# Performance work log

Measured on AMD Instinct MI355X. Metric: run time of the kernel, lower is better.

## Reference

```python
import jax, jax.numpy as jnp
import numpy as np

N_NODES = 100000
N_EDGES = 1600000
IN_DIM, HID_DIM, OUT_DIM = 128, 64, 64


def setup_inputs() -> dict:
    key = jax.random.key(0)
    ks = jax.random.split(key, 8)
    x = jax.random.normal(ks[0], (N_NODES, IN_DIM), dtype=jnp.float32)
    edge_index = jax.random.randint(ks[1], (2, N_EDGES), 0, N_NODES, dtype=jnp.int32)
    edge_weight = jax.random.uniform(ks[2], (N_EDGES,), dtype=jnp.float32)
    # GCNConv parameters (glorot-ish init)
    w1 = jax.random.normal(ks[3], (IN_DIM, HID_DIM), dtype=jnp.float32) / np.sqrt(IN_DIM)
    b1 = jnp.zeros((HID_DIM,), dtype=jnp.float32)
    w2 = jax.random.normal(ks[4], (HID_DIM, OUT_DIM), dtype=jnp.float32) / np.sqrt(HID_DIM)
    b2 = jnp.zeros((OUT_DIM,), dtype=jnp.float32)
    return {"x": x, "edge_index": edge_index, "edge_weight": edge_weight,
            "w1": w1, "b1": b1, "w2": w2, "b2": b2}


def _gcn_conv(h, src, dst, edge_weight, w, b, n_nodes):
    # GCNConv(normalize=False): linear transform, then edge-weighted scatter-add
    # (source_to_target flow: gather from src, scatter-sum into dst), then bias.
    h = h @ w                                   # [N, out]
    msg = h[src] * edge_weight[:, None]          # [E, out] irregular gather
    agg = jax.ops.segment_sum(msg, dst, num_segments=n_nodes)  # [N, out]
    return agg + b


def reference(x, edge_index, edge_weight, w1, b1, w2, b2):
    src, dst = edge_index[0], edge_index[1]
    n = x.shape[0]
    # Dropout is identity in eval mode (training=False).
    h = _gcn_conv(x, src, dst, edge_weight, w1, b1, n)
    h = jax.nn.relu(h)
    out = _gcn_conv(h, src, dst, edge_weight, w2, b2, n)
    return out
```

## Files before the change

### kernel.cpp

```cpp
#include <hip/hip_runtime.h>
#include <hip/hip_bf16.h>


#define N_NODES 100000
#define N_EDGES 1600000
#define NB1     391
#define T1      4096
#define NT1     391
#define CAP1    4706
#define GB1     782

typedef unsigned short ushort_t;
typedef unsigned int uint_t;
typedef __attribute__((ext_vector_type(8))) short bf16x8;
typedef __attribute__((ext_vector_type(4))) float floatx4;
typedef __attribute__((ext_vector_type(8))) ushort_t ushort8v;

static __device__ __forceinline__ float bf2f(ushort_t h) {
    return __uint_as_float(((uint_t)h) << 16);
}
static __device__ __forceinline__ ushort_t f2bf(float f) {
    uint_t u = __float_as_uint(f);
    u = (u + 0x7FFF + ((u >> 16) & 1)) >> 16;
    return (ushort_t)u;
}

__global__ __launch_bounds__(512) void k_init(int* __restrict__ gcursor)
{
    int t = threadIdx.x;
    if (t < NB1) gcursor[t] = t * CAP1;
}

__global__ __launch_bounds__(512) void k_p1g1(
    const int* __restrict__ src, const int* __restrict__ dst,
    const float* __restrict__ ew, int* __restrict__ gcursor,
    int2* __restrict__ recs1, int E,
    const float* __restrict__ X, const float* __restrict__ W,
    ushort_t* __restrict__ Y, int N)
{
    __shared__ __align__(16) char smem[52224];
    const int tid = threadIdx.x;

    if (blockIdx.x < NT1) {
        int* cnt     = (int*)smem;
        int* start   = cnt + NB1;
        int* cursor  = start + NB1;
        int* gb      = cursor + NB1;
        int* s       = (int*)(smem + 6256);
        int2* stg    = (int2*)(smem + 8304);
        ushort_t* sb = (ushort_t*)(smem + 41072);
        const int t = tid, b = blockIdx.x;

        if (t < NB1) cnt[t] = 0;
        __syncthreads();
        const int e0 = b * T1;
        const int e1 = min(E, e0 + T1);
        for (int e = e0 + t; e < e1; e += 512)
            atomicAdd(&cnt[dst[e] >> 8], 1);
        __syncthreads();
        const int v = (t < NB1) ? cnt[t] : 0;
        s[t] = v;
        #pragma unroll
        for (int off = 1; off < 512; off <<= 1) {
            __syncthreads();
            int a = (t >= off) ? s[t - off] : 0;
            __syncthreads();
            s[t] += a;
        }
        __syncthreads();
        if (t < NB1) {
            int st = s[t] - v;
            start[t]  = st;
            cursor[t] = st;
            gb[t]     = atomicAdd(&gcursor[t], v);
        }
        __syncthreads();
        for (int e = e0 + t; e < e1; e += 512) {
            int d  = dst[e];
            int bk = d >> 8;
            int p  = atomicAdd(&cursor[bk], 1);
            int2 r;
            r.x = ((d & 255) << 17) | src[e];
            r.y = __float_as_int(ew[e]);
            stg[p] = r;
            sb[p]  = (ushort_t)bk;
        }
        __syncthreads();
        const int n = e1 - e0;
        for (int i = t; i < n; i += 512) {
            int bk = sb[i];
            recs1[gb[bk] + (i - start[bk])] = stg[i];
        }
    } else {
        ushort_t* sA = (ushort_t*)smem;
        ushort_t* sB = (ushort_t*)(smem + 34816);
        const int b    = blockIdx.x - NT1;
        const int row0 = b * 128;

        for (int i = tid; i < 128 * 32; i += 512) {
            int r = i >> 5, c4 = (i & 31) * 4;
            int rg = row0 + r; if (rg > N - 1) rg = N - 1;
            float4 v = *(const float4*)(X + (size_t)rg * 128 + c4);
            ushort4 pk = make_ushort4(f2bf(v.x), f2bf(v.y), f2bf(v.z), f2bf(v.w));
            *(ushort4*)(sA + r * 136 + c4) = pk;
        }
        for (int i = tid; i < 128 * 16; i += 512) {
            int k = i >> 4, n4 = (i & 15) * 4;
            float4 v = *(const float4*)(W + (size_t)k * 64 + n4);
            sB[(n4 + 0) * 136 + k] = f2bf(v.x);
            sB[(n4 + 1) * 136 + k] = f2bf(v.y);
            sB[(n4 + 2) * 136 + k] = f2bf(v.z);
            sB[(n4 + 3) * 136 + k] = f2bf(v.w);
        }
        __syncthreads();

        const int wid = tid >> 6, lane = tid & 63;
        const int m = lane & 15, quad = lane >> 4;
        floatx4 acc[4] = {};

        #pragma unroll
        for (int ks = 0; ks < 4; ++ks) {
            bf16x8 a = *(const bf16x8*)(sA + (wid * 16 + m) * 136 + ks * 32 + quad * 8);
            #pragma unroll
            for (int nt = 0; nt < 4; ++nt) {
                bf16x8 bfr = *(const bf16x8*)(sB + (nt * 16 + m) * 136 + ks * 32 + quad * 8);
                acc[nt] = __builtin_amdgcn_mfma_f32_16x16x32_bf16(a, bfr, acc[nt], 0, 0, 0);
            }
        }
        __syncthreads();
        #pragma unroll
        for (int nt = 0; nt < 4; ++nt)
            #pragma unroll
            for (int r = 0; r < 4; ++r)
                sA[(wid * 16 + quad * 4 + r) * 72 + nt * 16 + m] = f2bf(acc[nt][r]);
        __syncthreads();
        for (int i = tid; i < 128 * 8; i += 512) {
            int rr = i >> 3, c8 = (i & 7) * 8;
            int rg = row0 + rr;
            if (rg < N)
                *(ushort8v*)(Y + (size_t)rg * 64 + c8) =
                    *(const ushort8v*)(sA + rr * 72 + c8);
        }
    }
}

__global__ __launch_bounds__(1024) void k_pass2(
    const int2* __restrict__ recs1, const int* __restrict__ gcursor,
    int2* __restrict__ recs2, int2* __restrict__ nodeinfo, int N)
{
    __shared__ int cnt[256];
    __shared__ int s[256];
    __shared__ int cursor[256];
    const int t = threadIdx.x, b = blockIdx.x;
    const int lo = b * CAP1;
    const int hi = gcursor[b];

    if (t < 256) cnt[t] = 0;
    __syncthreads();
    for (int j = lo + t; j < hi; j += 1024)
        atomicAdd(&cnt[((uint_t)recs1[j].x) >> 17], 1);
    __syncthreads();
    const int v = (t < 256) ? cnt[t] : 0;
    if (t < 256) s[t] = v;
    #pragma unroll
    for (int off = 1; off < 256; off <<= 1) {
        __syncthreads();
        int a = (t >= off && t < 256) ? s[t - off] : 0;
        __syncthreads();
        if (t < 256) s[t] += a;
    }
    __syncthreads();
    if (t < 256) {
        const int stl = s[t] - v;
        cursor[t] = stl;
        const int ng = b * 256 + t;
        if (ng < N) {
            int2 ni; ni.x = lo + stl; ni.y = v;
            nodeinfo[ng] = ni;
        }
    }
    __syncthreads();
    for (int j = lo + t; j < hi; j += 1024) {
        int2 r = recs1[j];
        int dl = ((uint_t)r.x) >> 17;
        int p  = atomicAdd(&cursor[dl], 1);
        int2 o;
        o.x = r.x & 0x1FFFF;
        o.y = r.y;
        recs2[lo + p] = o;
    }
}

__global__ __launch_bounds__(256) void k_gemm2(
    const ushort_t* __restrict__ X, const float* __restrict__ W,
    ushort_t* __restrict__ Y, int N)
{
    __shared__ ushort_t sA[64 * 72];
    __shared__ ushort_t sB[64 * 72];
    const int tid  = threadIdx.x;
    const int row0 = blockIdx.x * 64;

    for (int i = tid; i < 64 * 16; i += 256) {
        int r = i >> 4, c4 = (i & 15) * 4;
        int rg = row0 + r; if (rg > N - 1) rg = N - 1;
        *(ushort4*)(sA + r * 72 + c4) =
            *(const ushort4*)(X + (size_t)rg * 64 + c4);
    }
    for (int i = tid; i < 64 * 16; i += 256) {
        int k = i >> 4, n4 = (i & 15) * 4;
        float4 v = *(const float4*)(W + (size_t)k * 64 + n4);
        sB[(n4 + 0) * 72 + k] = f2bf(v.x);
        sB[(n4 + 1) * 72 + k] = f2bf(v.y);
        sB[(n4 + 2) * 72 + k] = f2bf(v.z);
        sB[(n4 + 3) * 72 + k] = f2bf(v.w);
    }
    __syncthreads();

    const int wid = tid >> 6, lane = tid & 63;
    const int m = lane & 15, quad = lane >> 4;
    floatx4 acc[4] = {};

    #pragma unroll
    for (int ks = 0; ks < 2; ++ks) {
        bf16x8 a = *(const bf16x8*)(sA + (wid * 16 + m) * 72 + ks * 32 + quad * 8);
        #pragma unroll
        for (int nt = 0; nt < 4; ++nt) {
            bf16x8 bfr = *(const bf16x8*)(sB + (nt * 16 + m) * 72 + ks * 32 + quad * 8);
            acc[nt] = __builtin_amdgcn_mfma_f32_16x16x32_bf16(a, bfr, acc[nt], 0, 0, 0);
        }
    }
    __syncthreads();
    #pragma unroll
    for (int nt = 0; nt < 4; ++nt)
        #pragma unroll
        for (int r = 0; r < 4; ++r)
            sA[(wid * 16 + quad * 4 + r) * 72 + nt * 16 + m] = f2bf(acc[nt][r]);
    __syncthreads();
    for (int i = tid; i < 64 * 8; i += 256) {
        int rr = i >> 3, c8 = (i & 7) * 8;
        int rg = row0 + rr;
        if (rg < N)
            *(ushort8v*)(Y + (size_t)rg * 64 + c8) =
                *(const ushort8v*)(sA + rr * 72 + c8);
    }
}

template<bool RELU, bool OUT_BF16>
__global__ __launch_bounds__(256) void k_gather(
    const ushort_t* __restrict__ H, const int2* __restrict__ recs,
    const int2* __restrict__ nodeinfo, const float* __restrict__ bias,
    void* __restrict__ out)
{
    const int wid  = threadIdx.x >> 6;
    const int lane = threadIdx.x & 63;
    const int n0   = (blockIdx.x * 4 + wid) * 2;
    const int n1   = n0 + 1;

    const int2 niA = nodeinfo[n0];
    const int2 niB = nodeinfo[n1];
    int baseA = niA.x; const int endA = niA.x + niA.y;
    int baseB = niB.x; const int endB = niB.x + niB.y;

    const int g  = lane >> 4;
    const int c4 = (lane & 15) * 4;

    float a0 = 0.f, a1 = 0.f, a2 = 0.f, a3 = 0.f;
    float b0 = 0.f, b1 = 0.f, b2 = 0.f, b3 = 0.f;

    while (baseA < endA || baseB < endB) {
        int mA = endA - baseA; if (mA > 64) mA = 64;
        int mB = endB - baseB; if (mB > 64) mB = 64;
        int2 rA = (mA > 0) ? recs[baseA + (lane < mA ? lane : mA - 1)]
                           : make_int2(0, 0);
        int2 rB = (mB > 0) ? recs[baseB + (lane < mB ? lane : mB - 1)]
                           : make_int2(0, 0);
        float wAf = __int_as_float(rA.y);
        float wBf = __int_as_float(rB.y);
        int mm = mA > mB ? mA : mB;
        #pragma unroll 4
        for (int jj = 0; jj < mm; jj += 4) {
            int idx = jj + g;
            int   sA = __shfl(rA.x, idx);
            float wA = __shfl(wAf, idx);
            int   sB = __shfl(rB.x, idx);
            float wB = __shfl(wBf, idx);
            if (idx >= mA) wA = 0.f;
            if (idx >= mB) wB = 0.f;
            ushort4 hA = *(const ushort4*)(H + (size_t)sA * 64 + c4);
            ushort4 hB = *(const ushort4*)(H + (size_t)sB * 64 + c4);
            a0 = fmaf(wA, bf2f(hA.x), a0);
            a1 = fmaf(wA, bf2f(hA.y), a1);
            a2 = fmaf(wA, bf2f(hA.z), a2);
            a3 = fmaf(wA, bf2f(hA.w), a3);
            b0 = fmaf(wB, bf2f(hB.x), b0);
            b1 = fmaf(wB, bf2f(hB.y), b1);
            b2 = fmaf(wB, bf2f(hB.z), b2);
            b3 = fmaf(wB, bf2f(hB.w), b3);
        }
        baseA += 64;
        baseB += 64;
    }
    a0 += __shfl_down(a0, 32); a1 += __shfl_down(a1, 32);
    a2 += __shfl_down(a2, 32); a3 += __shfl_down(a3, 32);
    b0 += __shfl_down(b0, 32); b1 += __shfl_down(b1, 32);
    b2 += __shfl_down(b2, 32); b3 += __shfl_down(b3, 32);
    a0 += __shfl_down(a0, 16); a1 += __shfl_down(a1, 16);
    a2 += __shfl_down(a2, 16); a3 += __shfl_down(a3, 16);
    b0 += __shfl_down(b0, 16); b1 += __shfl_down(b1, 16);
    b2 += __shfl_down(b2, 16); b3 += __shfl_down(b3, 16);

    if (lane < 16) {
        float4 bv = *(const float4*)(bias + c4);
        float vA0 = a0 + bv.x, vA1 = a1 + bv.y, vA2 = a2 + bv.z, vA3 = a3 + bv.w;
        float vB0 = b0 + bv.x, vB1 = b1 + bv.y, vB2 = b2 + bv.z, vB3 = b3 + bv.w;
        if (RELU) {
            vA0 = fmaxf(vA0, 0.f); vA1 = fmaxf(vA1, 0.f);
            vA2 = fmaxf(vA2, 0.f); vA3 = fmaxf(vA3, 0.f);
            vB0 = fmaxf(vB0, 0.f); vB1 = fmaxf(vB1, 0.f);
            vB2 = fmaxf(vB2, 0.f); vB3 = fmaxf(vB3, 0.f);
        }
        if (OUT_BF16) {
            *(ushort4*)((ushort_t*)out + (size_t)n0 * 64 + c4) =
                make_ushort4(f2bf(vA0), f2bf(vA1), f2bf(vA2), f2bf(vA3));
            *(ushort4*)((ushort_t*)out + (size_t)n1 * 64 + c4) =
                make_ushort4(f2bf(vB0), f2bf(vB1), f2bf(vB2), f2bf(vB3));
        } else {
            *(float4*)((float*)out + (size_t)n0 * 64 + c4) =
                make_float4(vA0, vA1, vA2, vA3);
            *(float4*)((float*)out + (size_t)n1 * 64 + c4) =
                make_float4(vB0, vB1, vB2, vB3);
        }
    }
}

extern "C" void kernel_launch(void* const* d_in, const int* in_sizes, int n_in,
                              void* d_out, int out_size, void* d_ws, size_t ws_size,
                              hipStream_t stream) {
    const float* x   = (const float*)d_in[0];
    const int*   ei  = (const int*)  d_in[1];
    const float* ew  = (const float*)d_in[2];
    const float* w1  = (const float*)d_in[3];
    const float* b1  = (const float*)d_in[4];
    const float* w2  = (const float*)d_in[5];
    const float* b2  = (const float*)d_in[6];
    float* out = (float*)d_out;

    const int N = N_NODES, E = N_EDGES;
    const int* src = ei;
    const int* dst = ei + E;

    char* p = (char*)d_ws;
    ushort_t* bufA   = (ushort_t*)p;  p += (size_t)N_NODES * 64 * 2;
    int2*     recs2  = (int2*)p;      p += (size_t)NB1 * CAP1 * 8;
    int2*     recs1  = (int2*)p;
    ushort_t* bufB   = (ushort_t*)p;  p += (size_t)NB1 * CAP1 * 8;
    int*      gcur   = (int*)p;       p += 2048;
    int2*     ninfo  = (int2*)p;      p += (size_t)N_NODES * 8;

    k_init <<<1, 512, 0, stream>>>(gcur);
    k_p1g1 <<<NT1 + GB1, 512, 0, stream>>>(src, dst, ew, gcur, recs1, E,
                                           x, w1, bufA, N);
    k_pass2<<<NB1, 1024, 0, stream>>>(recs1, gcur, recs2, ninfo, N);

    k_gather<true, true><<<N / 8, 256, 0, stream>>>(bufA, recs2, ninfo, b1, bufB);

    k_gemm2<<<(N + 63) / 64, 256, 0, stream>>>(bufB, w2, bufA, N);
    k_gather<false, false><<<N / 8, 256, 0, stream>>>(bufA, recs2, ninfo, b2, out);
}
```

Measured before the change: 232.6 us.

## Shrink shared memory in fused bucket/GEMM kernel to raise occupancy

```diff
diff --git a/kernel.cpp b/kernel.cpp
--- a/kernel.cpp
+++ b/kernel.cpp
@@ -5,8 +5,8 @@
 #define N_NODES 100000
 #define N_EDGES 1600000
 #define NB1     391
-#define T1      4096
-#define NT1     391
+#define T1      3072
+#define NT1     521
 #define CAP1    4706
 #define GB1     782
 
@@ -38,7 +38,7 @@
     const float* __restrict__ X, const float* __restrict__ W,
     ushort_t* __restrict__ Y, int N)
 {
-    __shared__ __align__(16) char smem[52224];
+    __shared__ __align__(16) char smem[37056];
     const int tid = threadIdx.x;
 
     if (blockIdx.x < NT1) {
@@ -46,10 +46,12 @@
         int* start   = cnt + NB1;
         int* cursor  = start + NB1;
         int* gb      = cursor + NB1;
-        int* s       = (int*)(smem + 6256);
-        int2* stg    = (int2*)(smem + 8304);
-        ushort_t* sb = (ushort_t*)(smem + 41072);
+        int* wsum    = (int*)(smem + 6256);
+        int* wexc    = wsum + 8;
+        int2* stg    = (int2*)(smem + 6336);
+        ushort_t* sb = (ushort_t*)(smem + 30912);
         const int t = tid, b = blockIdx.x;
+        const int lane = t & 63, wv = t >> 6;
 
         if (t < NB1) cnt[t] = 0;
         __syncthreads();
@@ -58,23 +60,35 @@
         for (int e = e0 + t; e < e1; e += 512)
             atomicAdd(&cnt[dst[e] >> 8], 1);
         __syncthreads();
+
         const int v = (t < NB1) ? cnt[t] : 0;
-        s[t] = v;
-        #pragma unroll
-        for (int off = 1; off < 512; off <<= 1) {
-            __syncthreads();
-            int a = (t >= off) ? s[t - off] : 0;
-            __syncthreads();
-            s[t] += a;
+        int x = v;
+        #pragma unroll
+        for (int off = 1; off < 64; off <<= 1) {
+            int y = __shfl_up(x, off);
+            if (lane >= off) x += y;
+        }
+        if (lane == 63) wsum[wv] = x;
+        __syncthreads();
+        if (t < 8) {
+            int w  = wsum[t];
+            int xx = w;
+            #pragma unroll
+            for (int off = 1; off < 8; off <<= 1) {
+                int y = __shfl_up(xx, off);
+                if (t >= off) xx += y;
+            }
+            wexc[t] = xx - w;
         }
         __syncthreads();
         if (t < NB1) {
-            int st = s[t] - v;
+            int st = x + wexc[wv] - v;
             start[t]  = st;
             cursor[t] = st;
             gb[t]     = atomicAdd(&gcursor[t], v);
         }
         __syncthreads();
+
         for (int e = e0 + t; e < e1; e += 512) {
             int d  = dst[e];
             int bk = d >> 8;
@@ -93,17 +107,10 @@
         }
     } else {
         ushort_t* sA = (ushort_t*)smem;
-        ushort_t* sB = (ushort_t*)(smem + 34816);
+        ushort_t* sB = (ushort_t*)(smem + 18432);
         const int b    = blockIdx.x - NT1;
         const int row0 = b * 128;
 
-        for (int i = tid; i < 128 * 32; i += 512) {
-            int r = i >> 5, c4 = (i & 31) * 4;
-            int rg = row0 + r; if (rg > N - 1) rg = N - 1;
-            float4 v = *(const float4*)(X + (size_t)rg * 128 + c4);
-            ushort4 pk = make_ushort4(f2bf(v.x), f2bf(v.y), f2bf(v.z), f2bf(v.w));
-            *(ushort4*)(sA + r * 136 + c4) = pk;
-        }
         for (int i = tid; i < 128 * 16; i += 512) {
             int k = i >> 4, n4 = (i & 15) * 4;
             float4 v = *(const float4*)(W + (size_t)k * 64 + n4);
@@ -112,6 +119,13 @@
             sB[(n4 + 2) * 136 + k] = f2bf(v.z);
             sB[(n4 + 3) * 136 + k] = f2bf(v.w);
         }
+        for (int i = tid; i < 128 * 16; i += 512) {
+            int r = i >> 4, c4 = (i & 15) * 4;
+            int rg = row0 + r; if (rg > N - 1) rg = N - 1;
+            float4 v = *(const float4*)(X + (size_t)rg * 128 + c4);
+            *(ushort4*)(sA + r * 72 + c4) =
+                make_ushort4(f2bf(v.x), f2bf(v.y), f2bf(v.z), f2bf(v.w));
+        }
         __syncthreads();
 
         const int wid = tid >> 6, lane = tid & 63;
@@ -119,11 +133,29 @@
         floatx4 acc[4] = {};
 
         #pragma unroll
-        for (int ks = 0; ks < 4; ++ks) {
-            bf16x8 a = *(const bf16x8*)(sA + (wid * 16 + m) * 136 + ks * 32 + quad * 8);
+        for (int ksl = 0; ksl < 2; ++ksl) {
+            bf16x8 a = *(const bf16x8*)(sA + (wid * 16 + m) * 72 + ksl * 32 + quad * 8);
             #pragma unroll
             for (int nt = 0; nt < 4; ++nt) {
-                bf16x8 bfr = *(const bf16x8*)(sB + (nt * 16 + m) * 136 + ks * 32 + quad * 8);
+                bf16x8 bfr = *(const bf16x8*)(sB + (nt * 16 + m) * 136 + ksl * 32 + quad * 8);
+                acc[nt] = __builtin_amdgcn_mfma_f32_16x16x32_bf16(a, bfr, acc[nt], 0, 0, 0);
+            }
+        }
+        __syncthreads();
+        for (int i = tid; i < 128 * 16; i += 512) {
+            int r = i >> 4, c4 = (i & 15) * 4;
+            int rg = row0 + r; if (rg > N - 1) rg = N - 1;
+            float4 v = *(const float4*)(X + (size_t)rg * 128 + 64 + c4);
+            *(ushort4*)(sA + r * 72 + c4) =
+                make_ushort4(f2bf(v.x), f2bf(v.y), f2bf(v.z), f2bf(v.w));
+        }
+        __syncthreads();
+        #pragma unroll
+        for (int ksl = 0; ksl < 2; ++ksl) {
+            bf16x8 a = *(const bf16x8*)(sA + (wid * 16 + m) * 72 + ksl * 32 + quad * 8);
+            #pragma unroll
+            for (int nt = 0; nt < 4; ++nt) {
+                bf16x8 bfr = *(const bf16x8*)(sB + (nt * 16 + m) * 136 + 64 + ksl * 32 + quad * 8);
                 acc[nt] = __builtin_amdgcn_mfma_f32_16x16x32_bf16(a, bfr, acc[nt], 0, 0, 0);
             }
         }
```

Measured after the change: 235.6 us. Within noise of the previous version (+1.3%).

## Fuse pass2, gathers and second GEMM into one cooperative persistent kernel

Applied to the files above, without the earlier changes.

```diff
diff --git a/kernel.cpp b/kernel.cpp
--- a/kernel.cpp
+++ b/kernel.cpp
@@ -1,5 +1,8 @@
 #include <hip/hip_runtime.h>
 #include <hip/hip_bf16.h>
+#include <hip/hip_cooperative_groups.h>
+
+namespace cg = cooperative_groups;
 
 
 #define N_NODES 100000
@@ -9,6 +12,7 @@
 #define NT1     391
 #define CAP1    4706
 #define GB1     782
+#define RESTB   768
 
 typedef unsigned short ushort_t;
 typedef unsigned int uint_t;
@@ -46,10 +50,12 @@
         int* start   = cnt + NB1;
         int* cursor  = start + NB1;
         int* gb      = cursor + NB1;
-        int* s       = (int*)(smem + 6256);
-        int2* stg    = (int2*)(smem + 8304);
-        ushort_t* sb = (ushort_t*)(smem + 41072);
+        int* wsum    = (int*)(smem + 6256);
+        int* wexc    = wsum + 8;
+        int2* stg    = (int2*)(smem + 6336);
+        ushort_t* sb = (ushort_t*)(smem + 39104);
         const int t = tid, b = blockIdx.x;
+        const int lane = t & 63, wv = t >> 6;
 
         if (t < NB1) cnt[t] = 0;
         __syncthreads();
@@ -58,23 +64,35 @@
         for (int e = e0 + t; e < e1; e += 512)
             atomicAdd(&cnt[dst[e] >> 8], 1);
         __syncthreads();
+
         const int v = (t < NB1) ? cnt[t] : 0;
-        s[t] = v;
+        int x = v;
         #pragma unroll
-        for (int off = 1; off < 512; off <<= 1) {
-            __syncthreads();
-            int a = (t >= off) ? s[t - off] : 0;
-            __syncthreads();
-            s[t] += a;
+        for (int off = 1; off < 64; off <<= 1) {
+            int y = __shfl_up(x, off);
+            if (lane >= off) x += y;
+        }
+        if (lane == 63) wsum[wv] = x;
+        __syncthreads();
+        if (t < 8) {
+            int w  = wsum[t];
+            int xx = w;
+            #pragma unroll
+            for (int off = 1; off < 8; off <<= 1) {
+                int y = __shfl_up(xx, off);
+                if (t >= off) xx += y;
+            }
+            wexc[t] = xx - w;
         }
         __syncthreads();
         if (t < NB1) {
-            int st = s[t] - v;
+            int st = x + wexc[wv] - v;
             start[t]  = st;
             cursor[t] = st;
             gb[t]     = atomicAdd(&gcursor[t], v);
         }
         __syncthreads();
+
         for (int e = e0 + t; e < e1; e += 512) {
             int d  = dst[e];
             int bk = d >> 8;
@@ -144,117 +162,15 @@
     }
 }
 
-__global__ __launch_bounds__(1024) void k_pass2(
-    const int2* __restrict__ recs1, const int* __restrict__ gcursor,
-    int2* __restrict__ recs2, int2* __restrict__ nodeinfo, int N)
-{
-    __shared__ int cnt[256];
-    __shared__ int s[256];
-    __shared__ int cursor[256];
-    const int t = threadIdx.x, b = blockIdx.x;
-    const int lo = b * CAP1;
-    const int hi = gcursor[b];
-
-    if (t < 256) cnt[t] = 0;
-    __syncthreads();
-    for (int j = lo + t; j < hi; j += 1024)
-        atomicAdd(&cnt[((uint_t)recs1[j].x) >> 17], 1);
-    __syncthreads();
-    const int v = (t < 256) ? cnt[t] : 0;
-    if (t < 256) s[t] = v;
-    #pragma unroll
-    for (int off = 1; off < 256; off <<= 1) {
-        __syncthreads();
-        int a = (t >= off && t < 256) ? s[t - off] : 0;
-        __syncthreads();
-        if (t < 256) s[t] += a;
-    }
-    __syncthreads();
-    if (t < 256) {
-        const int stl = s[t] - v;
-        cursor[t] = stl;
-        const int ng = b * 256 + t;
-        if (ng < N) {
-            int2 ni; ni.x = lo + stl; ni.y = v;
-            nodeinfo[ng] = ni;
-        }
-    }
-    __syncthreads();
-    for (int j = lo + t; j < hi; j += 1024) {
-        int2 r = recs1[j];
-        int dl = ((uint_t)r.x) >> 17;
-        int p  = atomicAdd(&cursor[dl], 1);
-        int2 o;
-        o.x = r.x & 0x1FFFF;
-        o.y = r.y;
-        recs2[lo + p] = o;
-    }
-}
-
-__global__ __launch_bounds__(256) void k_gemm2(
-    const ushort_t* __restrict__ X, const float* __restrict__ W,
-    ushort_t* __restrict__ Y, int N)
-{
-    __shared__ ushort_t sA[64 * 72];
-    __shared__ ushort_t sB[64 * 72];
-    const int tid  = threadIdx.x;
-    const int row0 = blockIdx.x * 64;
-
-    for (int i = tid; i < 64 * 16; i += 256) {
-        int r = i >> 4, c4 = (i & 15) * 4;
-        int rg = row0 + r; if (rg > N - 1) rg = N - 1;
-        *(ushort4*)(sA + r * 72 + c4) =
-            *(const ushort4*)(X + (size_t)rg * 64 + c4);
-    }
-    for (int i = tid; i < 64 * 16; i += 256) {
-        int k = i >> 4, n4 = (i & 15) * 4;
-        float4 v = *(const float4*)(W + (size_t)k * 64 + n4);
-        sB[(n4 + 0) * 72 + k] = f2bf(v.x);
-        sB[(n4 + 1) * 72 + k] = f2bf(v.y);
-        sB[(n4 + 2) * 72 + k] = f2bf(v.z);
-        sB[(n4 + 3) * 72 + k] = f2bf(v.w);
-    }
-    __syncthreads();
-
-    const int wid = tid >> 6, lane = tid & 63;
-    const int m = lane & 15, quad = lane >> 4;
-    floatx4 acc[4] = {};
-
-    #pragma unroll
-    for (int ks = 0; ks < 2; ++ks) {
-        bf16x8 a = *(const bf16x8*)(sA + (wid * 16 + m) * 72 + ks * 32 + quad * 8);
-        #pragma unroll
-        for (int nt = 0; nt < 4; ++nt) {
-            bf16x8 bfr = *(const bf16x8*)(sB + (nt * 16 + m) * 72 + ks * 32 + quad * 8);
-            acc[nt] = __builtin_amdgcn_mfma_f32_16x16x32_bf16(a, bfr, acc[nt], 0, 0, 0);
-        }
-    }
-    __syncthreads();
-    #pragma unroll
-    for (int nt = 0; nt < 4; ++nt)
-        #pragma unroll
-        for (int r = 0; r < 4; ++r)
-            sA[(wid * 16 + quad * 4 + r) * 72 + nt * 16 + m] = f2bf(acc[nt][r]);
-    __syncthreads();
-    for (int i = tid; i < 64 * 8; i += 256) {
-        int rr = i >> 3, c8 = (i & 7) * 8;
-        int rg = row0 + rr;
-        if (rg < N)
-            *(ushort8v*)(Y + (size_t)rg * 64 + c8) =
-                *(const ushort8v*)(sA + rr * 72 + c8);
-    }
-}
-
 template<bool RELU, bool OUT_BF16>
-__global__ __launch_bounds__(256) void k_gather(
+static __device__ __forceinline__ void gather_item(
+    int i, int wid, int lane,
     const ushort_t* __restrict__ H, const int2* __restrict__ recs,
     const int2* __restrict__ nodeinfo, const float* __restrict__ bias,
     void* __restrict__ out)
 {
-    const int wid  = threadIdx.x >> 6;
-    const int lane = threadIdx.x & 63;
-    const int n0   = (blockIdx.x * 4 + wid) * 2;
-    const int n1   = n0 + 1;
+    const int n0 = (i * 4 + wid) * 2;
+    const int n1 = n0 + 1;
 
     const int2 niA = nodeinfo[n0];
     const int2 niB = nodeinfo[n1];
@@ -333,6 +249,134 @@
     }
 }
 
+__global__ __launch_bounds__(256, 4) void k_rest(
+    const int2* __restrict__ recs1, const int* __restrict__ gcursor,
+    int2* __restrict__ recs2, int2* __restrict__ ninfo,
+    ushort_t* __restrict__ bufA,
+    const float* __restrict__ b1, ushort_t* __restrict__ bufB,
+    const float* __restrict__ w2, const float* __restrict__ b2,
+    float* __restrict__ out, int N)
+{
+    cg::grid_group grid = cg::this_grid();
+    __shared__ __align__(16) char smem[18432];
+    const int tid  = threadIdx.x;
+    const int wid  = tid >> 6;
+    const int lane = tid & 63;
+
+    {
+        int* cnt    = (int*)smem;
+        int* cursor = cnt + 256;
+        int* wsum   = cursor + 256;
+        int* wexc   = wsum + 8;
+        const int t = tid;
+        for (int b = blockIdx.x; b < NB1; b += gridDim.x) {
+            const int lo = b * CAP1;
+            const int hi = gcursor[b];
+            cnt[t] = 0;
+            __syncthreads();
+            for (int j = lo + t; j < hi; j += 256)
+                atomicAdd(&cnt[((uint_t)recs1[j].x) >> 17], 1);
+            __syncthreads();
+            const int v = cnt[t];
+            int x = v;
+            #pragma unroll
+            for (int off = 1; off < 64; off <<= 1) {
+                int y = __shfl_up(x, off);
+                if (lane >= off) x += y;
+            }
+            if (lane == 63) wsum[wid] = x;
+            __syncthreads();
+            if (t < 4) {
+                int w  = wsum[t];
+                int xx = w;
+                #pragma unroll
+                for (int off = 1; off < 4; off <<= 1) {
+                    int y = __shfl_up(xx, off);
+                    if (t >= off) xx += y;
+                }
+                wexc[t] = xx - w;
+            }
+            __syncthreads();
+            const int stl = x + wexc[wid] - v;
+            cursor[t] = stl;
+            const int ng = b * 256 + t;
+            if (ng < N) {
+                int2 ni; ni.x = lo + stl; ni.y = v;
+                ninfo[ng] = ni;
+            }
+            __syncthreads();
+            for (int j = lo + t; j < hi; j += 256) {
+                int2 r = recs1[j];
+                int dl = ((uint_t)r.x) >> 17;
+                int p  = atomicAdd(&cursor[dl], 1);
+                int2 o;
+                o.x = r.x & 0x1FFFF;
+                o.y = r.y;
+                recs2[lo + p] = o;
+            }
+            __syncthreads();
+        }
+    }
+    grid.sync();
+
+    for (int i = blockIdx.x; i < N_NODES / 8; i += gridDim.x)
+        gather_item<true, true>(i, wid, lane, bufA, recs2, ninfo, b1, bufB);
+    grid.sync();
+
+    {
+        ushort_t* sA = (ushort_t*)smem;
+        ushort_t* sB = (ushort_t*)(smem + 9216);
+        const int m = lane & 15, quad = lane >> 4;
+        for (int it = blockIdx.x; it < (N_NODES + 63) / 64; it += gridDim.x) {
+            const int row0 = it * 64;
+            for (int i = tid; i < 64 * 16; i += 256) {
+                int r = i >> 4, c4 = (i & 15) * 4;
+                int rg = row0 + r; if (rg > N - 1) rg = N - 1;
+                *(ushort4*)(sA + r * 72 + c4) =
+                    *(const ushort4*)(bufB + (size_t)rg * 64 + c4);
+            }
+            for (int i = tid; i < 64 * 16; i += 256) {
+                int k = i >> 4, n4 = (i & 15) * 4;
+                float4 v = *(const float4*)(w2 + (size_t)k * 64 + n4);
+                sB[(n4 + 0) * 72 + k] = f2bf(v.x);
+                sB[(n4 + 1) * 72 + k] = f2bf(v.y);
+                sB[(n4 + 2) * 72 + k] = f2bf(v.z);
+                sB[(n4 + 3) * 72 + k] = f2bf(v.w);
+            }
+            __syncthreads();
+            floatx4 acc[4] = {};
+            #pragma unroll
+            for (int ks = 0; ks < 2; ++ks) {
+                bf16x8 a = *(const bf16x8*)(sA + (wid * 16 + m) * 72 + ks * 32 + quad * 8);
+                #pragma unroll
+                for (int nt = 0; nt < 4; ++nt) {
+                    bf16x8 bfr = *(const bf16x8*)(sB + (nt * 16 + m) * 72 + ks * 32 + quad * 8);
+                    acc[nt] = __builtin_amdgcn_mfma_f32_16x16x32_bf16(a, bfr, acc[nt], 0, 0, 0);
+                }
+            }
+            __syncthreads();
+            #pragma unroll
+            for (int nt = 0; nt < 4; ++nt)
+                #pragma unroll
+                for (int r = 0; r < 4; ++r)
+                    sA[(wid * 16 + quad * 4 + r) * 72 + nt * 16 + m] = f2bf(acc[nt][r]);
+            __syncthreads();
+            for (int i = tid; i < 64 * 8; i += 256) {
+                int rr = i >> 3, c8 = (i & 7) * 8;
+                int rg = row0 + rr;
+                if (rg < N)
+                    *(ushort8v*)(bufA + (size_t)rg * 64 + c8) =
+                        *(const ushort8v*)(sA + rr * 72 + c8);
+            }
+            __syncthreads();
+        }
+    }
+    grid.sync();
+
+    for (int i = blockIdx.x; i < N_NODES / 8; i += gridDim.x)
+        gather_item<false, false>(i, wid, lane, bufA, recs2, ninfo, b2, out);
+}
+
 extern "C" void kernel_launch(void* const* d_in, const int* in_sizes, int n_in,
                               void* d_out, int out_size, void* d_ws, size_t ws_size,
                               hipStream_t stream) {
@@ -345,7 +389,7 @@
     const float* b2  = (const float*)d_in[6];
     float* out = (float*)d_out;
 
-    const int N = N_NODES, E = N_EDGES;
+    int N = N_NODES, E = N_EDGES;
     const int* src = ei;
     const int* dst = ei + E;
 
@@ -360,10 +404,12 @@
     k_init <<<1, 512, 0, stream>>>(gcur);
     k_p1g1 <<<NT1 + GB1, 512, 0, stream>>>(src, dst, ew, gcur, recs1, E,
                                            x, w1, bufA, N);
-    k_pass2<<<NB1, 1024, 0, stream>>>(recs1, gcur, recs2, ninfo, N);
-
-    k_gather<true, true><<<N / 8, 256, 0, stream>>>(bufA, recs2, ninfo, b1, bufB);
-
-    k_gemm2<<<(N + 63) / 64, 256, 0, stream>>>(bufB, w2, bufA, N);
-    k_gather<false, false><<<N / 8, 256, 0, stream>>>(bufA, recs2, ninfo, b2, out);
-}
+
+    void* args[] = {
+        (void*)&recs1, (void*)&gcur, (void*)&recs2, (void*)&ninfo,
+        (void*)&bufA,  (void*)&b1,   (void*)&bufB,
+        (void*)&w2,    (void*)&b2,   (void*)&out,   (void*)&N
+    };
+    hipLaunchCooperativeKernel((void*)k_rest, dim3(RESTB), dim3(256),
+                               args, 0, stream);
+}
```

Measured after the change: 557.4 us. 2.4x slower.
